# Optimization experiments

Measured on AMD Instinct MI355X. Metric: run time of the kernel, lower is better.

## Reference

```python
import jax, jax.numpy as jnp
import numpy as np


def setup_inputs() -> dict:
    key = jax.random.key(0)
    ks = jax.random.split(key, 7)
    B, T, I, H, O = 64, 2048, 32, 256, 32
    s = 0.05
    return {
        "x": jax.random.normal(ks[0], (B, T, I), dtype=jnp.float32),
        "W_ih": jax.random.normal(ks[1], (4 * H, I), dtype=jnp.float32) * s,
        "W_hh": jax.random.normal(ks[2], (4 * H, H), dtype=jnp.float32) * s,
        "b_ih": jax.random.normal(ks[3], (4 * H,), dtype=jnp.float32) * s,
        "b_hh": jax.random.normal(ks[4], (4 * H,), dtype=jnp.float32) * s,
        "fc_w": jax.random.normal(ks[5], (O, H), dtype=jnp.float32) * s,
        "fc_b": jax.random.normal(ks[6], (O,), dtype=jnp.float32) * s,
    }


def _lstm(x, W_ih, W_hh, b_ih, b_hh):
    # x: [B,T,I]; PyTorch gate order: i, f, g, o stacked along 4H axis.
    B = x.shape[0]
    H = W_hh.shape[1]
    # Precompute input contributions for all timesteps in one GEMM: [B,T,4H]
    xg = jnp.einsum('bti,gi->btg', x, W_ih) + b_ih + b_hh

    def step(carry, xg_t):
        h, c = carry  # [B,H] each
        gates = xg_t + h @ W_hh.T  # [B,4H]
        i, f, g, o = jnp.split(gates, 4, axis=-1)
        i = jax.nn.sigmoid(i)
        f = jax.nn.sigmoid(f)
        g = jnp.tanh(g)
        o = jax.nn.sigmoid(o)
        c = f * c + i * g
        h = o * jnp.tanh(c)
        return (h, c), h

    h0 = jnp.zeros((B, H), dtype=x.dtype)
    (_, _), hs = jax.lax.scan(step, (h0, h0), jnp.swapaxes(xg, 0, 1))
    return jnp.swapaxes(hs, 0, 1)  # [B,T,H]


def reference(x, W_ih, W_hh, b_ih, b_hh, fc_w, fc_b):
    out = _lstm(x, W_ih, W_hh, b_ih, b_hh)          # [B,T,H]
    # Conv1d(H, O, kernel_size=1) over channel dim == pointwise linear.
    return jnp.einsum('bth,oh->bto', out, fc_w) + fc_b  # [B,T,O]
```

## Files before the change

### kernel.cpp

```cpp
#include <hip/hip_runtime.h>
#include <cstdint>


#define B_  64
#define T_  2048
#define I_  32
#define H_  256
#define G4  1024
#define O_  32

typedef int v16i __attribute__((ext_vector_type(16)));
typedef int v4i  __attribute__((ext_vector_type(4)));
typedef unsigned int v4u __attribute__((ext_vector_type(4)));
typedef _Float16 h2_t __attribute__((ext_vector_type(2)));

#if __has_builtin(__builtin_amdgcn_sdot4)
__device__ __forceinline__ int dot4(int a, int b, int c) {
    return __builtin_amdgcn_sdot4(a, b, c, false);
}
#else
__device__ __forceinline__ int dot4(int a, int b, int c) {
    c += (int)(int8_t)(a)        * (int)(int8_t)(b);
    c += (int)(int8_t)(a >> 8)   * (int)(int8_t)(b >> 8);
    c += (int)(int8_t)(a >> 16)  * (int)(int8_t)(b >> 16);
    c += (int)(int8_t)(a >> 24)  * (int)(int8_t)(b >> 24);
    return c;
}
#endif

__device__ __forceinline__ float fdot2h(h2_t a, h2_t b, float c) {
#if __has_builtin(__builtin_amdgcn_fdot2)
    return __builtin_amdgcn_fdot2(a, b, c, false);
#else
    return c + (float)a[0] * (float)b[0] + (float)a[1] * (float)b[1];
#endif
}

__device__ __forceinline__ float wave64_max_bcast(float v) {
    int t;
    t = __builtin_amdgcn_update_dpp(__float_as_int(v), __float_as_int(v), 0x111, 0xf, 0xf, false);
    v = fmaxf(v, __int_as_float(t));
    t = __builtin_amdgcn_update_dpp(__float_as_int(v), __float_as_int(v), 0x112, 0xf, 0xf, false);
    v = fmaxf(v, __int_as_float(t));
    t = __builtin_amdgcn_update_dpp(__float_as_int(v), __float_as_int(v), 0x114, 0xf, 0xf, false);
    v = fmaxf(v, __int_as_float(t));
    t = __builtin_amdgcn_update_dpp(__float_as_int(v), __float_as_int(v), 0x118, 0xf, 0xf, false);
    v = fmaxf(v, __int_as_float(t));
    t = __builtin_amdgcn_update_dpp(__float_as_int(v), __float_as_int(v), 0x142, 0xa, 0xf, false);
    v = fmaxf(v, __int_as_float(t));
    t = __builtin_amdgcn_update_dpp(__float_as_int(v), __float_as_int(v), 0x143, 0xc, 0xf, false);
    v = fmaxf(v, __int_as_float(t));
    return __int_as_float(__builtin_amdgcn_readlane(__float_as_int(v), 63));
}

__device__ __forceinline__ float halfwave_sum31(float v) {
    int t;
    t = __builtin_amdgcn_update_dpp(0, __float_as_int(v), 0x111, 0xf, 0xf, true); v += __int_as_float(t);
    t = __builtin_amdgcn_update_dpp(0, __float_as_int(v), 0x112, 0xf, 0xf, true); v += __int_as_float(t);
    t = __builtin_amdgcn_update_dpp(0, __float_as_int(v), 0x114, 0xf, 0xf, true); v += __int_as_float(t);
    t = __builtin_amdgcn_update_dpp(0, __float_as_int(v), 0x118, 0xf, 0xf, true); v += __int_as_float(t);
    t = __builtin_amdgcn_update_dpp(0, __float_as_int(v), 0x142, 0xa, 0xf, true); v += __int_as_float(t);
    return v;
}

#define QWHH_OFF 0
#define QWIH_OFF 262144
#define S1_OFF   327680
#define S2_OFF   331776
#define BIAS_OFF 335872
#define XQ_OFF   339968
#define XS_OFF   8728576
#define HBUF_OFF 9252864
#define HREC_STRIDE 320
#define HSLOTS 2049

__device__ __forceinline__ uint32_t pack_q(int q0, int q1, int q2, int q3) {
    return  ((uint32_t)(uint8_t)(int8_t)q0)
          | (((uint32_t)(uint8_t)(int8_t)q1) << 8)
          | (((uint32_t)(uint8_t)(int8_t)q2) << 16)
          | (((uint32_t)(uint8_t)(int8_t)q3) << 24);
}

__device__ __forceinline__ int clamp127(int v) {
    return v < -127 ? -127 : (v > 127 ? 127 : v);
}

__global__ __launch_bounds__(64) void prep_w(
    const float* __restrict__ Whh, const float* __restrict__ Wih,
    const float* __restrict__ bih, const float* __restrict__ bhh,
    uint32_t* __restrict__ qwhh, uint32_t* __restrict__ qwih,
    float* __restrict__ s1, float* __restrict__ s2, float* __restrict__ bias)
{
    const int r = blockIdx.x;
    const int l = threadIdx.x;

    const float4 wv = ((const float4*)(Whh + r * H_))[l];
    float m = fmaxf(fmaxf(fabsf(wv.x), fabsf(wv.y)), fmaxf(fabsf(wv.z), fabsf(wv.w)));
    #pragma unroll
    for (int s = 1; s < 64; s <<= 1) m = fmaxf(m, __shfl_xor(m, s, 64));
    const float S1 = fmaxf(m, 1e-20f) / 127.f;

    float xm = (l < I_) ? fabsf(Wih[r * I_ + l]) : 0.f;
    #pragma unroll
    for (int s = 1; s < 64; s <<= 1) xm = fmaxf(xm, __shfl_xor(xm, s, 64));
    const float S2 = fmaxf(xm, 1e-20f) / 127.f;

    {
        const float r1 = 1.f / S1;
        qwhh[l * G4 + r] = pack_q(
            clamp127((int)rintf(wv.x * r1)), clamp127((int)rintf(wv.y * r1)),
            clamp127((int)rintf(wv.z * r1)), clamp127((int)rintf(wv.w * r1)));
    }
    if (l < 8) {
        const float4 xw = ((const float4*)(Wih + r * I_))[l];
        const float r2 = 1.f / S2;
        qwih[l * G4 + r] = pack_q(
            clamp127((int)rintf(xw.x * r2)), clamp127((int)rintf(xw.y * r2)),
            clamp127((int)rintf(xw.z * r2)), clamp127((int)rintf(xw.w * r2)));
    } else if (l < 16) {
        const int j = l - 8;
        const float4 xw = ((const float4*)(Wih + r * I_))[j];
        const float r2 = 1.f / S2;
        float v0 = xw.x * r2, v1 = xw.y * r2, v2 = xw.z * r2, v3 = xw.w * r2;
        int a0 = clamp127((int)rintf(v0)), a1 = clamp127((int)rintf(v1));
        int a2 = clamp127((int)rintf(v2)), a3 = clamp127((int)rintf(v3));
        qwih[(8 + j) * G4 + r] = pack_q(
            clamp127((int)rintf((v0 - (float)a0) * 127.f)),
            clamp127((int)rintf((v1 - (float)a1) * 127.f)),
            clamp127((int)rintf((v2 - (float)a2) * 127.f)),
            clamp127((int)rintf((v3 - (float)a3) * 127.f)));
    }
    if (l == 0) { s1[r] = S1; s2[r] = S2; bias[r] = bih[r] + bhh[r]; }
}

__global__ __launch_bounds__(256) void prep_x(
    const float* __restrict__ x, uint32_t* __restrict__ xq, float* __restrict__ xs)
{
    __shared__ float xb[64 * 32];
    const int base = blockIdx.x * 64 * 32;
    for (int i = threadIdx.x; i < 2048; i += 256) xb[i] = x[base + i];
    __syncthreads();
    const int t = threadIdx.x;
    if (t < 64) {
        float m = 0.f;
        for (int k = 0; k < 32; k++) m = fmaxf(m, fabsf(xb[t * 32 + k]));
        const float S = fmaxf(m, 1e-20f) / 127.f;
        const int row = blockIdx.x * 64 + t;
        xs[row] = S;
        const float rS = 1.f / S;
        for (int j = 0; j < 8; j++) {
            int qa[4], qb[4];
            for (int e = 0; e < 4; e++) {
                float v = xb[t * 32 + j * 4 + e] * rS;
                int a = clamp127((int)rintf(v));
                int b = clamp127((int)rintf((v - (float)a) * 127.f));
                qa[e] = a; qb[e] = b;
            }
            xq[row * 16 + j]     = pack_q(qa[0], qa[1], qa[2], qa[3]);
            xq[row * 16 + 8 + j] = pack_q(qb[0], qb[1], qb[2], qb[3]);
        }
    }
}

__device__ __forceinline__ float xdots(v4u x0, v4u x1, v4u x2, v4u x3, float sx,
                                       const uint32_t* wA, const uint32_t* wB,
                                       float S2, float bias_r) {
    int aA = 0, aM = 0;
    #pragma unroll
    for (int j = 0; j < 4; j++) {
        aA = dot4((int)wA[j],     (int)x0[j], aA);
        aM = dot4((int)wA[j],     (int)x2[j], aM);
        aM = dot4((int)wB[j],     (int)x0[j], aM);
        aA = dot4((int)wA[4 + j], (int)x1[j], aA);
        aM = dot4((int)wA[4 + j], (int)x3[j], aM);
        aM = dot4((int)wB[4 + j], (int)x1[j], aM);
    }
    return ((float)aA + (float)aM * (1.f / 127.f)) * (S2 * sx) + bias_r;
}

__global__ __launch_bounds__(1024, 4) void lstm_main(
    const uint32_t* __restrict__ qwhh, const uint32_t* __restrict__ qwih,
    const float* __restrict__ s1v, const float* __restrict__ s2v,
    const float* __restrict__ biasv,
    const uint32_t* __restrict__ xq, const float* __restrict__ xs,
    const float* __restrict__ fcw, const float* __restrict__ fcb,
    char* __restrict__ hbuf, float* __restrict__ out)
{
    const int b   = blockIdx.x;
    const int tid = threadIdx.x;

    __shared__ float    gbuf[768];
    __shared__ uint32_t hf16[128];

    uint32_t w[64], wA[8], wB[8];
    #pragma unroll
    for (int d = 0; d < 64; d++) w[d] = qwhh[d * G4 + tid];
    #pragma unroll
    for (int j = 0; j < 8; j++) { wA[j] = qwih[j * G4 + tid]; wB[j] = qwih[(8 + j) * G4 + tid]; }
    const float S1 = s1v[tid], S2 = s2v[tid], bias_r = biasv[tid];

    const int o_ = tid >> 5, kc = tid & 31;
    h2_t fw[4];
    {
        const float* fr = fcw + o_ * H_ + kc * 8;
        #pragma unroll
        for (int j = 0; j < 4; j++) {
            h2_t p; p[0] = (_Float16)fr[2 * j]; p[1] = (_Float16)fr[2 * j + 1];
            fw[j] = p;
        }
    }
    const float fcb_v = fcb[o_];

    char* hb = hbuf + (size_t)b * (HSLOTS * HREC_STRIDE);
    if (tid < H_) hb[2048 * HREC_STRIDE + tid] = 0;
    if (tid >= 256 && tid < 260) ((float*)(hb + 2048 * HREC_STRIDE + 256))[tid - 256] = 0.f;

    const uint32_t* xqb  = xq + (size_t)(b * T_) * 16;
    const float*    xsb  = xs + (size_t)(b * T_);
    float*          outb = out + (size_t)(b * T_) * O_;

    float c_state = 0.f;
    float x_part;
    {
        const v4u x0 = *(const v4u*)(xqb);     const v4u x1 = *(const v4u*)(xqb + 4);
        const v4u x2 = *(const v4u*)(xqb + 8); const v4u x3 = *(const v4u*)(xqb + 12);
        x_part = xdots(x0, x1, x2, x3, xsb[0], wA, wB, S2, bias_r);
    }

    __syncthreads();

    for (int t = 0; t < T_; t++) {
        const uint32_t slot = (t == 0) ? 2048u : ((uint32_t)(t * 1993) & 2047u);
        const char* hrec = hb + (size_t)slot * HREC_STRIDE;
        v16i h0, h1, h2, h3; v4i scv;
        asm volatile("s_load_dwordx16 %0, %5, 0x0\n\t"
                     "s_load_dwordx16 %1, %5, 0x40\n\t"
                     "s_load_dwordx16 %2, %5, 0x80\n\t"
                     "s_load_dwordx16 %3, %5, 0xc0\n\t"
                     "s_load_dwordx4  %4, %5, 0x100"
                     : "=&s"(h0), "=&s"(h1), "=&s"(h2), "=&s"(h3), "=&s"(scv)
                     : "s"(hrec)
                     : "memory");

        const int tn = (t + 1 < T_) ? (t + 1) : t;
        const uint32_t* px = xqb + (size_t)tn * 16;
        const v4u x0 = *(const v4u*)(px);     const v4u x1 = *(const v4u*)(px + 4);
        const v4u x2 = *(const v4u*)(px + 8); const v4u x3 = *(const v4u*)(px + 12);
        const float sx = xsb[tn];

        if (t > 0) {
            const v4u hv = *(const v4u*)(&hf16[4 * kc]);
            union { uint32_t u; h2_t h; } u0, u1, u2, u3;
            u0.u = hv[0]; u1.u = hv[1]; u2.u = hv[2]; u3.u = hv[3];
            float acc = 0.f;
            acc = fdot2h(fw[0], u0.h, acc);
            acc = fdot2h(fw[1], u1.h, acc);
            acc = fdot2h(fw[2], u2.h, acc);
            acc = fdot2h(fw[3], u3.h, acc);
            acc = halfwave_sum31(acc);
            if ((tid & 31) == 31) outb[(t - 1) * O_ + o_] = acc + fcb_v;
        }

        asm volatile("s_waitcnt lgkmcnt(0)"
                     : "+s"(h0), "+s"(h1), "+s"(h2), "+s"(h3), "+s"(scv)
                     :
                     : "memory");

        int a0 = 0, a1 = 0, a2 = 0, a3 = 0;
        #pragma unroll
        for (int d = 0; d < 16; d++) {
            a0 = dot4((int)w[d],      h0[d], a0);
            a1 = dot4((int)w[16 + d], h1[d], a1);
            a2 = dot4((int)w[32 + d], h2[d], a2);
            a3 = dot4((int)w[48 + d], h3[d], a3);
        }
        const float hsum = (float)a0 * __int_as_float(scv[0])
                         + (float)a1 * __int_as_float(scv[1])
                         + (float)a2 * __int_as_float(scv[2])
                         + (float)a3 * __int_as_float(scv[3]);
        const float gate = hsum * S1 + x_part;

        if (tid >= 256) gbuf[tid - 256] = gate;
        __syncthreads();

        const uint32_t wslot = (uint32_t)((t + 1) * 1993) & 2047u;
        char* hw = hb + (size_t)wslot * HREC_STRIDE;
        if (tid < H_) {
            const float gi = gate;
            const float gf = gbuf[tid];
            const float gg = gbuf[256 + tid];
            const float go = gbuf[512 + tid];
            const float i_ = 1.f / (1.f + __expf(-gi));
            const float f_ = 1.f / (1.f + __expf(-gf));
            const float g_ = 2.f / (1.f + __expf(-2.f * gg)) - 1.f;
            const float oo = 1.f / (1.f + __expf(-go));
            c_state = f_ * c_state + i_ * g_;
            const float tc = 2.f / (1.f + __expf(-2.f * c_state)) - 1.f;
            const float hval = oo * tc;
            ((_Float16*)hf16)[tid] = (_Float16)hval;

            float m = wave64_max_bcast(fabsf(hval));
            m = fmaxf(m, 1e-12f);
            const float rq = 127.f / m;
            const int q = clamp127((int)rintf(hval * rq));
            hw[tid] = (char)(int8_t)q;
            if ((tid & 63) == 0)
                ((float*)(hw + 256))[tid >> 6] = m * (1.f / 127.f);
        }

        x_part = xdots(x0, x1, x2, x3, sx, wA, wB, S2, bias_r);

        __syncthreads();
    }

    {
        const v4u hv = *(const v4u*)(&hf16[4 * kc]);
        union { uint32_t u; h2_t h; } u0, u1, u2, u3;
        u0.u = hv[0]; u1.u = hv[1]; u2.u = hv[2]; u3.u = hv[3];
        float acc = 0.f;
        acc = fdot2h(fw[0], u0.h, acc);
        acc = fdot2h(fw[1], u1.h, acc);
        acc = fdot2h(fw[2], u2.h, acc);
        acc = fdot2h(fw[3], u3.h, acc);
        acc = halfwave_sum31(acc);
        if ((tid & 31) == 31) outb[(T_ - 1) * O_ + o_] = acc + fcb_v;
    }
}

extern "C" void kernel_launch(void* const* d_in, const int* in_sizes, int n_in,
                              void* d_out, int out_size, void* d_ws, size_t ws_size,
                              hipStream_t stream) {
    const float* x    = (const float*)d_in[0];
    const float* Wih  = (const float*)d_in[1];
    const float* Whh  = (const float*)d_in[2];
    const float* bih  = (const float*)d_in[3];
    const float* bhh  = (const float*)d_in[4];
    const float* fcw  = (const float*)d_in[5];
    const float* fcb  = (const float*)d_in[6];
    float* out = (float*)d_out;

    char* ws = (char*)d_ws;
    uint32_t* qwhh = (uint32_t*)(ws + QWHH_OFF);
    uint32_t* qwih = (uint32_t*)(ws + QWIH_OFF);
    float*    s1   = (float*)(ws + S1_OFF);
    float*    s2   = (float*)(ws + S2_OFF);
    float*    bias = (float*)(ws + BIAS_OFF);
    uint32_t* xq   = (uint32_t*)(ws + XQ_OFF);
    float*    xs   = (float*)(ws + XS_OFF);
    char*     hbuf = ws + HBUF_OFF;

    prep_w<<<G4, 64, 0, stream>>>(Whh, Wih, bih, bhh, qwhh, qwih, s1, s2, bias);
    prep_x<<<(B_ * T_) / 64, 256, 0, stream>>>(x, xq, xs);
    lstm_main<<<B_, 1024, 0, stream>>>(qwhh, qwih, s1, s2, bias, xq, xs,
                                       fcw, fcb, hbuf, out);
}
```

Baseline: 3.711 ms.

## Interleave two batch sequences per block to overlap pointwise and matvec phases

```diff
diff --git a/kernel.cpp b/kernel.cpp
--- a/kernel.cpp
+++ b/kernel.cpp
@@ -162,20 +162,38 @@
     }
 }
 
-__device__ __forceinline__ float xdots(v4u x0, v4u x1, v4u x2, v4u x3, float sx,
-                                       const uint32_t* wA, const uint32_t* wB,
-                                       float S2, float bias_r) {
+__device__ __forceinline__ float x_contrib(const uint32_t* pxq, const float* pxs,
+                                           const uint32_t* wA, const uint32_t* wB,
+                                           float S2, float bias_r) {
+    v16i xv; int sxi;
+    asm volatile("s_load_dwordx16 %0, %2, 0x0\n\t"
+                 "s_load_dword %1, %3, 0x0\n\t"
+                 "s_waitcnt lgkmcnt(0)"
+                 : "=&s"(xv), "=&s"(sxi)
+                 : "s"(pxq), "s"(pxs)
+                 : "memory");
     int aA = 0, aM = 0;
     #pragma unroll
-    for (int j = 0; j < 4; j++) {
-        aA = dot4((int)wA[j],     (int)x0[j], aA);
-        aM = dot4((int)wA[j],     (int)x2[j], aM);
-        aM = dot4((int)wB[j],     (int)x0[j], aM);
-        aA = dot4((int)wA[4 + j], (int)x1[j], aA);
-        aM = dot4((int)wA[4 + j], (int)x3[j], aM);
-        aM = dot4((int)wB[4 + j], (int)x1[j], aM);
-    }
-    return ((float)aA + (float)aM * (1.f / 127.f)) * (S2 * sx) + bias_r;
+    for (int j = 0; j < 8; j++) {
+        aA = dot4((int)wA[j], xv[j],     aA);
+        aM = dot4((int)wA[j], xv[8 + j], aM);
+        aM = dot4((int)wB[j], xv[j],     aM);
+    }
+    return ((float)aA + (float)aM * (1.f / 127.f)) * (S2 * __int_as_float(sxi)) + bias_r;
+}
+
+__device__ __forceinline__ void fc_step(const uint32_t* hfbuf, float* outp, int trow,
+                                        const h2_t* fw, float fcb_v, int o_, int kc) {
+    const v4u hv = *(const v4u*)(&hfbuf[4 * kc]);
+    union { uint32_t u; h2_t h; } u0, u1, u2, u3;
+    u0.u = hv[0]; u1.u = hv[1]; u2.u = hv[2]; u3.u = hv[3];
+    float acc = 0.f;
+    acc = fdot2h(fw[0], u0.h, acc);
+    acc = fdot2h(fw[1], u1.h, acc);
+    acc = fdot2h(fw[2], u2.h, acc);
+    acc = fdot2h(fw[3], u3.h, acc);
+    acc = halfwave_sum31(acc);
+    if (kc == 31) outp[trow * O_ + o_] = acc + fcb_v;
 }
 
 __global__ __launch_bounds__(1024, 4) void lstm_main(
@@ -186,11 +204,14 @@
     const float* __restrict__ fcw, const float* __restrict__ fcb,
     char* __restrict__ hbuf, float* __restrict__ out)
 {
-    const int b   = blockIdx.x;
+    const int blk = blockIdx.x;
+    const int b0  = 2 * blk, b1 = 2 * blk + 1;
     const int tid = threadIdx.x;
 
-    __shared__ float    gbuf[768];
-    __shared__ uint32_t hf16[128];
+    __shared__ float    gbuf0[768];
+    __shared__ float    gbuf1[768];
+    __shared__ uint32_t hf16a[128];
+    __shared__ uint32_t hf16b[128];
 
     uint32_t w[64], wA[8], wB[8];
     #pragma unroll
@@ -211,120 +232,183 @@
     }
     const float fcb_v = fcb[o_];
 
-    char* hb = hbuf + (size_t)b * (HSLOTS * HREC_STRIDE);
-    if (tid < H_) hb[2048 * HREC_STRIDE + tid] = 0;
-    if (tid >= 256 && tid < 260) ((float*)(hb + 2048 * HREC_STRIDE + 256))[tid - 256] = 0.f;
-
-    const uint32_t* xqb  = xq + (size_t)(b * T_) * 16;
-    const float*    xsb  = xs + (size_t)(b * T_);
-    float*          outb = out + (size_t)(b * T_) * O_;
+    char* hb0 = hbuf + (size_t)b0 * (HSLOTS * HREC_STRIDE);
+    char* hb1 = hbuf + (size_t)b1 * (HSLOTS * HREC_STRIDE);
+    {
+        char* z0 = hb0 + 2048 * HREC_STRIDE;
+        char* z1 = hb1 + 2048 * HREC_STRIDE;
+        if (tid < 256)      z0[tid] = 0;
+        else if (tid < 512) z1[tid - 256] = 0;
+        else if (tid < 516) ((float*)(z0 + 256))[tid - 512] = 0.f;
+        else if (tid < 520) ((float*)(z1 + 256))[tid - 516] = 0.f;
+    }
+
+    const uint32_t* xq0 = xq + (size_t)(b0 * T_) * 16;
+    const float*    xs0 = xs + (size_t)(b0 * T_);
+    const uint32_t* xq1 = xq + (size_t)(b1 * T_) * 16;
+    const float*    xs1 = xs + (size_t)(b1 * T_);
+    float* out0 = out + (size_t)(b0 * T_) * O_;
+    float* out1 = out + (size_t)(b1 * T_) * O_;
 
     float c_state = 0.f;
-    float x_part;
-    {
-        const v4u x0 = *(const v4u*)(xqb);     const v4u x1 = *(const v4u*)(xqb + 4);
-        const v4u x2 = *(const v4u*)(xqb + 8); const v4u x3 = *(const v4u*)(xqb + 12);
-        x_part = xdots(x0, x1, x2, x3, xsb[0], wA, wB, S2, bias_r);
-    }
+    float gate0 = 0.f, gate1 = 0.f;
+    float xp0, xp1;
+
+    xp0 = x_contrib(xq0, xs0, wA, wB, S2, bias_r);
 
     __syncthreads();
 
     for (int t = 0; t < T_; t++) {
-        const uint32_t slot = (t == 0) ? 2048u : ((uint32_t)(t * 1993) & 2047u);
-        const char* hrec = hb + (size_t)slot * HREC_STRIDE;
-        v16i h0, h1, h2, h3; v4i scv;
-        asm volatile("s_load_dwordx16 %0, %5, 0x0\n\t"
-                     "s_load_dwordx16 %1, %5, 0x40\n\t"
-                     "s_load_dwordx16 %2, %5, 0x80\n\t"
-                     "s_load_dwordx16 %3, %5, 0xc0\n\t"
-                     "s_load_dwordx4  %4, %5, 0x100"
-                     : "=&s"(h0), "=&s"(h1), "=&s"(h2), "=&s"(h3), "=&s"(scv)
-                     : "s"(hrec)
-                     : "memory");
-
-        const int tn = (t + 1 < T_) ? (t + 1) : t;
-        const uint32_t* px = xqb + (size_t)tn * 16;
-        const v4u x0 = *(const v4u*)(px);     const v4u x1 = *(const v4u*)(px + 4);
-        const v4u x2 = *(const v4u*)(px + 8); const v4u x3 = *(const v4u*)(px + 12);
-        const float sx = xsb[tn];
-
-        if (t > 0) {
-            const v4u hv = *(const v4u*)(&hf16[4 * kc]);
-            union { uint32_t u; h2_t h; } u0, u1, u2, u3;
-            u0.u = hv[0]; u1.u = hv[1]; u2.u = hv[2]; u3.u = hv[3];
-            float acc = 0.f;
-            acc = fdot2h(fw[0], u0.h, acc);
-            acc = fdot2h(fw[1], u1.h, acc);
-            acc = fdot2h(fw[2], u2.h, acc);
-            acc = fdot2h(fw[3], u3.h, acc);
-            acc = halfwave_sum31(acc);
-            if ((tid & 31) == 31) outb[(t - 1) * O_ + o_] = acc + fcb_v;
+        {
+            const uint32_t slot = (t == 0) ? 2048u : ((uint32_t)(t * 1993) & 2047u);
+            const char* hrec = hb0 + (size_t)slot * HREC_STRIDE;
+            v16i h0, h1, h2, h3; v4i scv;
+            asm volatile("s_load_dwordx16 %0, %5, 0x0\n\t"
+                         "s_load_dwordx16 %1, %5, 0x40\n\t"
+                         "s_load_dwordx16 %2, %5, 0x80\n\t"
+                         "s_load_dwordx16 %3, %5, 0xc0\n\t"
+                         "s_load_dwordx4  %4, %5, 0x100"
+                         : "=&s"(h0), "=&s"(h1), "=&s"(h2), "=&s"(h3), "=&s"(scv)
+                         : "s"(hrec)
+                         : "memory");
+
+            if (t > 0)
+                fc_step(hf16a, out0, t - 1, fw, fcb_v, o_, kc);
+
+            asm volatile("s_waitcnt lgkmcnt(0)"
+                         : "+s"(h0), "+s"(h1), "+s"(h2), "+s"(h3), "+s"(scv)
+                         :
+                         : "memory");
+
+            int a0 = 0, a1 = 0, a2 = 0, a3 = 0;
+            #pragma unroll
+            for (int d = 0; d < 16; d++) {
+                a0 = dot4((int)w[d],      h0[d], a0);
+                a1 = dot4((int)w[16 + d], h1[d], a1);
+                a2 = dot4((int)w[32 + d], h2[d], a2);
+                a3 = dot4((int)w[48 + d], h3[d], a3);
+            }
+            const float hsum = (float)a0 * __int_as_float(scv[0])
+                             + (float)a1 * __int_as_float(scv[1])
+                             + (float)a2 * __int_as_float(scv[2])
+                             + (float)a3 * __int_as_float(scv[3]);
+            gate0 = hsum * S1 + xp0;
+
+            if (tid >= 256) gbuf0[tid - 256] = gate0;
+
+            if (t > 0 && tid >= 256 && tid < 512) {
+                const int rr = tid - 256;
+                const float gi = gbuf1[rr];
+                const float gf = gate1;
+                const float gg = gbuf1[256 + rr];
+                const float go = gbuf1[512 + rr];
+                const float i_ = 1.f / (1.f + __expf(-gi));
+                const float f_ = 1.f / (1.f + __expf(-gf));
+                const float g_ = 2.f / (1.f + __expf(-2.f * gg)) - 1.f;
+                const float oo = 1.f / (1.f + __expf(-go));
+                c_state = f_ * c_state + i_ * g_;
+                const float tc = 2.f / (1.f + __expf(-2.f * c_state)) - 1.f;
+                const float hval = oo * tc;
+                ((_Float16*)hf16b)[rr] = (_Float16)hval;
+
+                float m = wave64_max_bcast(fabsf(hval));
+                m = fmaxf(m, 1e-12f);
+                const int q = clamp127((int)rintf(hval * (127.f / m)));
+                char* hw = hb1 + (size_t)((uint32_t)(t * 1993) & 2047u) * HREC_STRIDE;
+                hw[rr] = (char)(int8_t)q;
+                if ((rr & 63) == 0)
+                    ((float*)(hw + 256))[rr >> 6] = m * (1.f / 127.f);
+            }
+
+            xp1 = x_contrib(xq1 + (size_t)t * 16, xs1 + t, wA, wB, S2, bias_r);
+
+            __syncthreads();
         }
-
-        asm volatile("s_waitcnt lgkmcnt(0)"
-                     : "+s"(h0), "+s"(h1), "+s"(h2), "+s"(h3), "+s"(scv)
-                     :
-                     : "memory");
-
-        int a0 = 0, a1 = 0, a2 = 0, a3 = 0;
-        #pragma unroll
-        for (int d = 0; d < 16; d++) {
-            a0 = dot4((int)w[d],      h0[d], a0);
-            a1 = dot4((int)w[16 + d], h1[d], a1);
-            a2 = dot4((int)w[32 + d], h2[d], a2);
-            a3 = dot4((int)w[48 + d], h3[d], a3);
+        {
+            const uint32_t slot = (t == 0) ? 2048u : ((uint32_t)(t * 1993) & 2047u);
+            const char* hrec = hb1 + (size_t)slot * HREC_STRIDE;
+            v16i h0, h1, h2, h3; v4i scv;
+            asm volatile("s_load_dwordx16 %0, %5, 0x0\n\t"
+                         "s_load_dwordx16 %1, %5, 0x40\n\t"
+                         "s_load_dwordx16 %2, %5, 0x80\n\t"
+                         "s_load_dwordx16 %3, %5, 0xc0\n\t"
+                         "s_load_dwordx4  %4, %5, 0x100"
+                         : "=&s"(h0), "=&s"(h1), "=&s"(h2), "=&s"(h3), "=&s"(scv)
+                         : "s"(hrec)
+                         : "memory");
+
+            if (t > 0)
+                fc_step(hf16b, out1, t - 1, fw, fcb_v, o_, kc);
+
+            asm volatile("s_waitcnt lgkmcnt(0)"
+                         : "+s"(h0), "+s"(h1), "+s"(h2), "+s"(h3), "+s"(scv)
+                         :
+                         : "memory");
+
+            int a0 = 0, a1 = 0, a2 = 0, a3 = 0;
+            #pragma unroll
+            for (int d = 0; d < 16; d++) {
+                a0 = dot4((int)w[d],      h0[d], a0);
+                a1 = dot4((int)w[16 + d], h1[d], a1);
+                a2 = dot4((int)w[32 + d], h2[d], a2);
+                a3 = dot4((int)w[48 + d], h3[d], a3);
+            }
+            const float hsum = (float)a0 * __int_as_float(scv[0])
+                             + (float)a1 * __int_as_float(scv[1])
+                             + (float)a2 * __int_as_float(scv[2])
+                             + (float)a3 * __int_as_float(scv[3]);
+            gate1 = hsum * S1 + xp1;
+
+            if (tid < 256)       gbuf1[tid] = gate1;
+            else if (tid >= 512) gbuf1[tid - 256] = gate1;
+
+            if (tid < 256) {
+                const float gi = gate0;
+                const float gf = gbuf0[tid];
+                const float gg = gbuf0[256 + tid];
+                const float go = gbuf0[512 + tid];
+                const float i_ = 1.f / (1.f + __expf(-gi));
+                const float f_ = 1.f / (1.f + __expf(-gf));
+                const float g_ = 2.f / (1.f + __expf(-2.f * gg)) - 1.f;
+                const float oo = 1.f / (1.f + __expf(-go));
+                c_state = f_ * c_state + i_ * g_;
+                const float tc = 2.f / (1.f + __expf(-2.f * c_state)) - 1.f;
+                const float hval = oo * tc;
+                ((_Float16*)hf16a)[tid] = (_Float16)hval;
+
+                float m = wave64_max_bcast(fabsf(hval));
+                m = fmaxf(m, 1e-12f);
+                const int q = clamp127((int)rintf(hval * (127.f / m)));
+                char* hw = hb0 + (size_t)((uint32_t)((t + 1) * 1993) & 2047u) * HREC_STRIDE;
+                hw[tid] = (char)(int8_t)q;
+                if ((tid & 63) == 0)
+                    ((float*)(hw + 256))[tid >> 6] = m * (1.f / 127.f);
+            }
+
+            const int tn = (t + 1 < T_) ? (t + 1) : t;
+            xp0 = x_contrib(xq0 + (size_t)tn * 16, xs0 + tn, wA, wB, S2, bias_r);
+
+            __syncthreads();
         }
-        const float hsum = (float)a0 * __int_as_float(scv[0])
-                         + (float)a1 * __int_as_float(scv[1])
-                         + (float)a2 * __int_as_float(scv[2])
-                         + (float)a3 * __int_as_float(scv[3]);
-        const float gate = hsum * S1 + x_part;
-
-        if (tid >= 256) gbuf[tid - 256] = gate;
-        __syncthreads();
-
-        const uint32_t wslot = (uint32_t)((t + 1) * 1993) & 2047u;
-        char* hw = hb + (size_t)wslot * HREC_STRIDE;
-        if (tid < H_) {
-            const float gi = gate;
-            const float gf = gbuf[tid];
-            const float gg = gbuf[256 + tid];
-            const float go = gbuf[512 + tid];
-            const float i_ = 1.f / (1.f + __expf(-gi));
-            const float f_ = 1.f / (1.f + __expf(-gf));
-            const float g_ = 2.f / (1.f + __expf(-2.f * gg)) - 1.f;
-            const float oo = 1.f / (1.f + __expf(-go));
-            c_state = f_ * c_state + i_ * g_;
-            const float tc = 2.f / (1.f + __expf(-2.f * c_state)) - 1.f;
-            const float hval = oo * tc;
-            ((_Float16*)hf16)[tid] = (_Float16)hval;
-
-            float m = wave64_max_bcast(fabsf(hval));
-            m = fmaxf(m, 1e-12f);
-            const float rq = 127.f / m;
-            const int q = clamp127((int)rintf(hval * rq));
-            hw[tid] = (char)(int8_t)q;
-            if ((tid & 63) == 0)
-                ((float*)(hw + 256))[tid >> 6] = m * (1.f / 127.f);
-        }
-
-        x_part = xdots(x0, x1, x2, x3, sx, wA, wB, S2, bias_r);
-
-        __syncthreads();
-    }
-
-    {
-        const v4u hv = *(const v4u*)(&hf16[4 * kc]);
-        union { uint32_t u; h2_t h; } u0, u1, u2, u3;
-        u0.u = hv[0]; u1.u = hv[1]; u2.u = hv[2]; u3.u = hv[3];
-        float acc = 0.f;
-        acc = fdot2h(fw[0], u0.h, acc);
-        acc = fdot2h(fw[1], u1.h, acc);
-        acc = fdot2h(fw[2], u2.h, acc);
-        acc = fdot2h(fw[3], u3.h, acc);
-        acc = halfwave_sum31(acc);
-        if ((tid & 31) == 31) outb[(T_ - 1) * O_ + o_] = acc + fcb_v;
-    }
+    }
+
+    if (tid >= 256 && tid < 512) {
+        const int rr = tid - 256;
+        const float gi = gbuf1[rr];
+        const float gf = gate1;
+        const float gg = gbuf1[256 + rr];
+        const float go = gbuf1[512 + rr];
+        const float i_ = 1.f / (1.f + __expf(-gi));
+        const float f_ = 1.f / (1.f + __expf(-gf));
+        const float g_ = 2.f / (1.f + __expf(-2.f * gg)) - 1.f;
+        const float oo = 1.f / (1.f + __expf(-go));
+        c_state = f_ * c_state + i_ * g_;
+        const float tc = 2.f / (1.f + __expf(-2.f * c_state)) - 1.f;
+        ((_Float16*)hf16b)[rr] = (_Float16)(oo * tc);
+    }
+    fc_step(hf16a, out0, T_ - 1, fw, fcb_v, o_, kc);
+    __syncthreads();
+    fc_step(hf16b, out1, T_ - 1, fw, fcb_v, o_, kc);
 }
 
 extern "C" void kernel_launch(void* const* d_in, const int* in_sizes, int n_in,
@@ -351,6 +435,6 @@
 
     prep_w<<<G4, 64, 0, stream>>>(Whh, Wih, bih, bhh, qwhh, qwih, s1, s2, bias);
     prep_x<<<(B_ * T_) / 64, 256, 0, stream>>>(x, xq, xs);
-    lstm_main<<<B_, 1024, 0, stream>>>(qwhh, qwih, s1, s2, bias, xq, xs,
-                                       fcw, fcb, hbuf, out);
-}
+    lstm_main<<<B_ / 2, 1024, 0, stream>>>(qwhh, qwih, s1, s2, bias, xq, xs,
+                                           fcw, fcb, hbuf, out);
+}
```

Result: slower. 6.530 ms (+76.0%).

## Remap gate rows so each wave owns all four gates, dropping one barrier

Applied to the files above, without the earlier changes.

```diff
diff --git a/kernel.cpp b/kernel.cpp
--- a/kernel.cpp
+++ b/kernel.cpp
@@ -10,7 +10,6 @@
 #define O_  32
 
 typedef int v16i __attribute__((ext_vector_type(16)));
-typedef int v4i  __attribute__((ext_vector_type(4)));
 typedef unsigned int v4u __attribute__((ext_vector_type(4)));
 typedef _Float16 h2_t __attribute__((ext_vector_type(2)));
 
@@ -162,20 +161,38 @@
     }
 }
 
-__device__ __forceinline__ float xdots(v4u x0, v4u x1, v4u x2, v4u x3, float sx,
-                                       const uint32_t* wA, const uint32_t* wB,
-                                       float S2, float bias_r) {
+__device__ __forceinline__ float x_contrib(const uint32_t* pxq, const float* pxs,
+                                           const uint32_t* wA, const uint32_t* wB,
+                                           float S2, float bias_r) {
+    v16i xv; int sxi;
+    asm volatile("s_load_dwordx16 %0, %2, 0x0\n\t"
+                 "s_load_dword %1, %3, 0x0\n\t"
+                 "s_waitcnt lgkmcnt(0)"
+                 : "=&s"(xv), "=&s"(sxi)
+                 : "s"(pxq), "s"(pxs)
+                 : "memory");
     int aA = 0, aM = 0;
     #pragma unroll
-    for (int j = 0; j < 4; j++) {
-        aA = dot4((int)wA[j],     (int)x0[j], aA);
-        aM = dot4((int)wA[j],     (int)x2[j], aM);
-        aM = dot4((int)wB[j],     (int)x0[j], aM);
-        aA = dot4((int)wA[4 + j], (int)x1[j], aA);
-        aM = dot4((int)wA[4 + j], (int)x3[j], aM);
-        aM = dot4((int)wB[4 + j], (int)x1[j], aM);
-    }
-    return ((float)aA + (float)aM * (1.f / 127.f)) * (S2 * sx) + bias_r;
+    for (int j = 0; j < 8; j++) {
+        aA = dot4((int)wA[j], xv[j],     aA);
+        aM = dot4((int)wA[j], xv[8 + j], aM);
+        aM = dot4((int)wB[j], xv[j],     aM);
+    }
+    return ((float)aA + (float)aM * (1.f / 127.f)) * (S2 * __int_as_float(sxi)) + bias_r;
+}
+
+__device__ __forceinline__ void fc_step(const uint32_t* hfbuf, float* outp, int trow,
+                                        const h2_t* fw, float fcb_v, int o_, int kc) {
+    const v4u hv = *(const v4u*)(&hfbuf[4 * kc]);
+    union { uint32_t u; h2_t h; } u0, u1, u2, u3;
+    u0.u = hv[0]; u1.u = hv[1]; u2.u = hv[2]; u3.u = hv[3];
+    float acc = 0.f;
+    acc = fdot2h(fw[0], u0.h, acc);
+    acc = fdot2h(fw[1], u1.h, acc);
+    acc = fdot2h(fw[2], u2.h, acc);
+    acc = fdot2h(fw[3], u3.h, acc);
+    acc = halfwave_sum31(acc);
+    if (kc == 31) outp[trow * O_ + o_] = acc + fcb_v;
 }
 
 __global__ __launch_bounds__(1024, 4) void lstm_main(
@@ -188,16 +205,20 @@
 {
     const int b   = blockIdx.x;
     const int tid = threadIdx.x;
-
-    __shared__ float    gbuf[768];
-    __shared__ uint32_t hf16[128];
+    const int wv  = tid >> 6;
+    const int ln  = tid & 63;
+    const int G   = ln >> 4;
+    const int r16 = ln & 15;
+    const int grow = G * 256 + wv * 16 + r16;
+
+    __shared__ uint32_t hf16[2][128];
 
     uint32_t w[64], wA[8], wB[8];
     #pragma unroll
-    for (int d = 0; d < 64; d++) w[d] = qwhh[d * G4 + tid];
-    #pragma unroll
-    for (int j = 0; j < 8; j++) { wA[j] = qwih[j * G4 + tid]; wB[j] = qwih[(8 + j) * G4 + tid]; }
-    const float S1 = s1v[tid], S2 = s2v[tid], bias_r = biasv[tid];
+    for (int d = 0; d < 64; d++) w[d] = qwhh[d * G4 + grow];
+    #pragma unroll
+    for (int j = 0; j < 8; j++) { wA[j] = qwih[j * G4 + grow]; wB[j] = qwih[(8 + j) * G4 + grow]; }
+    const float S1 = s1v[grow], S2 = s2v[grow], bias_r = biasv[grow];
 
     const int o_ = tid >> 5, kc = tid & 31;
     h2_t fw[4];
@@ -212,119 +233,112 @@
     const float fcb_v = fcb[o_];
 
     char* hb = hbuf + (size_t)b * (HSLOTS * HREC_STRIDE);
-    if (tid < H_) hb[2048 * HREC_STRIDE + tid] = 0;
-    if (tid >= 256 && tid < 260) ((float*)(hb + 2048 * HREC_STRIDE + 256))[tid - 256] = 0.f;
+    {
+        char* z = hb + 2048 * HREC_STRIDE;
+        if (tid < 256)      z[tid] = 0;
+        else if (tid < 272) ((uint32_t*)(z + 256))[tid - 256] = 0;
+    }
 
     const uint32_t* xqb  = xq + (size_t)(b * T_) * 16;
     const float*    xsb  = xs + (size_t)(b * T_);
     float*          outb = out + (size_t)(b * T_) * O_;
 
     float c_state = 0.f;
-    float x_part;
-    {
-        const v4u x0 = *(const v4u*)(xqb);     const v4u x1 = *(const v4u*)(xqb + 4);
-        const v4u x2 = *(const v4u*)(xqb + 8); const v4u x3 = *(const v4u*)(xqb + 12);
-        x_part = xdots(x0, x1, x2, x3, xsb[0], wA, wB, S2, bias_r);
-    }
+    float xp = x_contrib(xqb, xsb, wA, wB, S2, bias_r);
 
     __syncthreads();
 
     for (int t = 0; t < T_; t++) {
         const uint32_t slot = (t == 0) ? 2048u : ((uint32_t)(t * 1993) & 2047u);
         const char* hrec = hb + (size_t)slot * HREC_STRIDE;
-        v16i h0, h1, h2, h3; v4i scv;
+        v16i h0, h1, h2, h3, scv;
         asm volatile("s_load_dwordx16 %0, %5, 0x0\n\t"
                      "s_load_dwordx16 %1, %5, 0x40\n\t"
                      "s_load_dwordx16 %2, %5, 0x80\n\t"
                      "s_load_dwordx16 %3, %5, 0xc0\n\t"
-                     "s_load_dwordx4  %4, %5, 0x100"
+                     "s_load_dwordx16 %4, %5, 0x100"
                      : "=&s"(h0), "=&s"(h1), "=&s"(h2), "=&s"(h3), "=&s"(scv)
                      : "s"(hrec)
                      : "memory");
 
-        const int tn = (t + 1 < T_) ? (t + 1) : t;
-        const uint32_t* px = xqb + (size_t)tn * 16;
-        const v4u x0 = *(const v4u*)(px);     const v4u x1 = *(const v4u*)(px + 4);
-        const v4u x2 = *(const v4u*)(px + 8); const v4u x3 = *(const v4u*)(px + 12);
-        const float sx = xsb[tn];
-
-        if (t > 0) {
-            const v4u hv = *(const v4u*)(&hf16[4 * kc]);
-            union { uint32_t u; h2_t h; } u0, u1, u2, u3;
-            u0.u = hv[0]; u1.u = hv[1]; u2.u = hv[2]; u3.u = hv[3];
-            float acc = 0.f;
-            acc = fdot2h(fw[0], u0.h, acc);
-            acc = fdot2h(fw[1], u1.h, acc);
-            acc = fdot2h(fw[2], u2.h, acc);
-            acc = fdot2h(fw[3], u3.h, acc);
-            acc = halfwave_sum31(acc);
-            if ((tid & 31) == 31) outb[(t - 1) * O_ + o_] = acc + fcb_v;
-        }
+        if (t > 0)
+            fc_step(&hf16[(t - 1) & 1][0], outb, t - 1, fw, fcb_v, o_, kc);
 
         asm volatile("s_waitcnt lgkmcnt(0)"
                      : "+s"(h0), "+s"(h1), "+s"(h2), "+s"(h3), "+s"(scv)
                      :
                      : "memory");
 
-        int a0 = 0, a1 = 0, a2 = 0, a3 = 0;
-        #pragma unroll
-        for (int d = 0; d < 16; d++) {
-            a0 = dot4((int)w[d],      h0[d], a0);
-            a1 = dot4((int)w[16 + d], h1[d], a1);
-            a2 = dot4((int)w[32 + d], h2[d], a2);
-            a3 = dot4((int)w[48 + d], h3[d], a3);
-        }
-        const float hsum = (float)a0 * __int_as_float(scv[0])
-                         + (float)a1 * __int_as_float(scv[1])
-                         + (float)a2 * __int_as_float(scv[2])
-                         + (float)a3 * __int_as_float(scv[3]);
-        const float gate = hsum * S1 + x_part;
-
-        if (tid >= 256) gbuf[tid - 256] = gate;
-        __syncthreads();
+        float hs0 = 0.f, hs1 = 0.f, hs2 = 0.f, hs3 = 0.f;
+        #pragma unroll
+        for (int g = 0; g < 4; g++) {
+            int a = 0;
+            #pragma unroll
+            for (int j = 0; j < 4; j++) a = dot4((int)w[4 * g + j], h0[4 * g + j], a);
+            hs0 = fmaf((float)a, __int_as_float(scv[g]), hs0);
+        }
+        #pragma unroll
+        for (int g = 0; g < 4; g++) {
+            int a = 0;
+            #pragma unroll
+            for (int j = 0; j < 4; j++) a = dot4((int)w[16 + 4 * g + j], h1[4 * g + j], a);
+            hs1 = fmaf((float)a, __int_as_float(scv[4 + g]), hs1);
+        }
+        #pragma unroll
+        for (int g = 0; g < 4; g++) {
+            int a = 0;
+            #pragma unroll
+            for (int j = 0; j < 4; j++) a = dot4((int)w[32 + 4 * g + j], h2[4 * g + j], a);
+            hs2 = fmaf((float)a, __int_as_float(scv[8 + g]), hs2);
+        }
+        #pragma unroll
+        for (int g = 0; g < 4; g++) {
+            int a = 0;
+            #pragma unroll
+            for (int j = 0; j < 4; j++) a = dot4((int)w[48 + 4 * g + j], h3[4 * g + j], a);
+            hs3 = fmaf((float)a, __int_as_float(scv[12 + g]), hs3);
+        }
+        const float gate = ((hs0 + hs1) + (hs2 + hs3)) * S1 + xp;
+
+        const float vB = __shfl_xor(gate, 16, 64);
+        const float vC = __shfl_xor(gate, 32, 64);
+        const float vD = __shfl_xor(gate, 48, 64);
+        const bool s0 = (G & 1), s1b = (G & 2);
+        const float p00 = s0 ? vB : gate, p01 = s0 ? gate : vB;
+        const float p10 = s0 ? vD : vC,   p11 = s0 ? vC : vD;
+        const float gi = s1b ? p10 : p00;
+        const float gf = s1b ? p11 : p01;
+        const float gg = s1b ? p00 : p10;
+        const float go = s1b ? p01 : p11;
+
+        const float i_ = 1.f / (1.f + __expf(-gi));
+        const float f_ = 1.f / (1.f + __expf(-gf));
+        const float g_ = 2.f / (1.f + __expf(-2.f * gg)) - 1.f;
+        const float oo = 1.f / (1.f + __expf(-go));
+        c_state = f_ * c_state + i_ * g_;
+        const float tc = 2.f / (1.f + __expf(-2.f * c_state)) - 1.f;
+        const float hval = oo * tc;
 
         const uint32_t wslot = (uint32_t)((t + 1) * 1993) & 2047u;
         char* hw = hb + (size_t)wslot * HREC_STRIDE;
-        if (tid < H_) {
-            const float gi = gate;
-            const float gf = gbuf[tid];
-            const float gg = gbuf[256 + tid];
-            const float go = gbuf[512 + tid];
-            const float i_ = 1.f / (1.f + __expf(-gi));
-            const float f_ = 1.f / (1.f + __expf(-gf));
-            const float g_ = 2.f / (1.f + __expf(-2.f * gg)) - 1.f;
-            const float oo = 1.f / (1.f + __expf(-go));
-            c_state = f_ * c_state + i_ * g_;
-            const float tc = 2.f / (1.f + __expf(-2.f * c_state)) - 1.f;
-            const float hval = oo * tc;
-            ((_Float16*)hf16)[tid] = (_Float16)hval;
-
-            float m = wave64_max_bcast(fabsf(hval));
-            m = fmaxf(m, 1e-12f);
-            const float rq = 127.f / m;
-            const int q = clamp127((int)rintf(hval * rq));
-            hw[tid] = (char)(int8_t)q;
-            if ((tid & 63) == 0)
-                ((float*)(hw + 256))[tid >> 6] = m * (1.f / 127.f);
-        }
-
-        x_part = xdots(x0, x1, x2, x3, sx, wA, wB, S2, bias_r);
+        float m = wave64_max_bcast(fabsf(hval));
+        m = fmaxf(m, 1e-12f);
+        const float rq = 127.f / m;
+        const int q = clamp127((int)rintf(hval * rq));
+        if (G == 0) {
+            hw[wv * 16 + r16] = (char)(int8_t)q;
+            ((_Float16*)&hf16[t & 1][0])[wv * 16 + r16] = (_Float16)hval;
+        }
+        if (ln == 0)
+            ((float*)(hw + 256))[wv] = m * (1.f / 127.f);
+
+        const int tn = (t + 1 < T_) ? (t + 1) : t;
+        xp = x_contrib(xqb + (size_t)tn * 16, xsb + tn, wA, wB, S2, bias_r);
 
         __syncthreads();
     }
 
-    {
-        const v4u hv = *(const v4u*)(&hf16[4 * kc]);
-        union { uint32_t u; h2_t h; } u0, u1, u2, u3;
-        u0.u = hv[0]; u1.u = hv[1]; u2.u = hv[2]; u3.u = hv[3];
-        float acc = 0.f;
-        acc = fdot2h(fw[0], u0.h, acc);
-        acc = fdot2h(fw[1], u1.h, acc);
-        acc = fdot2h(fw[2], u2.h, acc);
-        acc = fdot2h(fw[3], u3.h, acc);
-        acc = halfwave_sum31(acc);
-        if ((tid & 31) == 31) outb[(T_ - 1) * O_ + o_] = acc + fcb_v;
-    }
+    fc_step(&hf16[(T_ - 1) & 1][0], outb, T_ - 1, fw, fcb_v, o_, kc);
 }
 
 extern "C" void kernel_launch(void* const* d_in, const int* in_sizes, int n_in,
```

After: 5.395 ms. 1.45x slower.
